# Kernel optimization log

Measured on AMD Instinct MI355X. Metric: run time of the kernel, lower is better.

## Reference

```python
import jax, jax.numpy as jnp
import numpy as np

H = 12
D_K = 64
NEG = -1e9
EPS = 1e-6
SQRT_2_PI = float(np.sqrt(2.0 / np.pi))


def gelu_tanh(x):
    return 0.5 * x * (1.0 + jnp.tanh(SQRT_2_PI * (x + 0.044715 * x * x * x)))


def layernorm(x, a, b):
    # torch std is unbiased (ddof=1); note original adds eps to std, not var
    mean = jnp.mean(x, axis=-1, keepdims=True)
    n = x.shape[-1]
    var = jnp.sum((x - mean) ** 2, axis=-1, keepdims=True) / (n - 1)
    std = jnp.sqrt(var)
    return a * (x - mean) / (std + EPS) + b


def setup_inputs() -> dict:
    key = jax.random.key(0)
    ks = jax.random.split(key, 16)
    B, S, D, F = 8, 1024, 768, 3072
    s = 0.02
    inp = {
        "x": jax.random.normal(ks[0], (B, S, D), jnp.float32),
        "mask": jnp.ones((B, 1, 1, S), jnp.int32),
        "Wq": jax.random.normal(ks[1], (D, D), jnp.float32) * s,
        "bq": jnp.zeros((D,), jnp.float32),
        "Wk": jax.random.normal(ks[2], (D, D), jnp.float32) * s,
        "bk": jnp.zeros((D,), jnp.float32),
        "Wv": jax.random.normal(ks[3], (D, D), jnp.float32) * s,
        "bv": jnp.zeros((D,), jnp.float32),
        "Wo": jax.random.normal(ks[4], (D, D), jnp.float32) * s,
        "bo": jnp.zeros((D,), jnp.float32),
        "W1": jax.random.normal(ks[5], (D, F), jnp.float32) * s,
        "b1": jnp.zeros((F,), jnp.float32),
        "W2": jax.random.normal(ks[6], (F, D), jnp.float32) * s,
        "b2": jnp.zeros((D,), jnp.float32),
        "ln1_a": jnp.ones((D,), jnp.float32),
        "ln1_b": jnp.ones((D,), jnp.float32),
        "ln2_a": jnp.ones((D,), jnp.float32),
        "ln2_b": jnp.ones((D,), jnp.float32),
    }
    return inp


def reference(x, mask, Wq, bq, Wk, bk, Wv, bv, Wo, bo, W1, b1, W2, b2,
              ln1_a, ln1_b, ln2_a, ln2_b):
    B, S, D = x.shape
    # QKV projections -> [B, H, S, d_k]
    def split_heads(t):
        return t.reshape(B, S, H, D_K).transpose(0, 2, 1, 3)
    q = split_heads(x @ Wq + bq)
    k = split_heads(x @ Wk + bk)
    v = split_heads(x @ Wv + bv)
    scores = jnp.einsum("bhqd,bhkd->bhqk", q, k) / jnp.sqrt(jnp.float32(D_K))
    scores = jnp.where(mask == 0, jnp.float32(NEG), scores)
    p = jax.nn.softmax(scores, axis=-1)
    attn = jnp.einsum("bhqk,bhkd->bhqd", p, v)
    attn = attn.transpose(0, 2, 1, 3).reshape(B, S, D)
    attn_out = attn @ Wo + bo
    out1 = layernorm(x + attn_out, ln1_a, ln1_b)
    ffn = gelu_tanh(out1 @ W1 + b1) @ W2 + b2
    out2 = layernorm(out1 + ffn, ln2_a, ln2_b)
    return out2
```

## Files before the change

kernel.cpp:

```cpp
#include <hip/hip_runtime.h>
#include <hip/hip_bf16.h>
#include <math.h>

#define BB 8
#define SS 1024
#define DD 768
#define FF 3072
#define HH 12
#define DK 64

typedef __bf16 bf16;
typedef __attribute__((ext_vector_type(8))) __bf16 bf16x8;
typedef __attribute__((ext_vector_type(4))) __bf16 bf16x4;
typedef __attribute__((ext_vector_type(4))) float f32x4;

#define AS1 __attribute__((address_space(1)))
#define AS3 __attribute__((address_space(3)))

#define EXP2_SCALE 0.18033688011112042f
#define NLOG2E2    -2.8853900817779268f

__device__ __forceinline__ float gelu_fast(float x) {
    const float u = 0.7978845608028654f * (x + 0.044715f * x * x * x);
    const float e = __builtin_amdgcn_exp2f(u * NLOG2E2);
    return x * __builtin_amdgcn_rcpf(1.0f + e);
}

template<int BN, int OUTB, int GELU_F, int RESID>
__global__ __launch_bounds__(256) void gemm_bf16(
    const bf16* __restrict__ A, const bf16* __restrict__ Bt,
    const float* __restrict__ bias, const float* __restrict__ R,
    void* __restrict__ Cout, int M, int N, int K)
{
    constexpr int NTJ   = BN / 32;
    constexpr int BITER = (BN * 8) / 256;

    __shared__ bf16x8 As[1024];
    __shared__ bf16x8 Bs[BN * 8];

    const int t    = threadIdx.x;
    const int wave = t >> 6;
    const int lane = t & 63;
    const int mtiles = M >> 7;
    const int m0 = (blockIdx.x % mtiles) * 128;
    const int n0 = (blockIdx.x / mtiles) * BN;
    const int wm = (wave >> 1) * 64;
    const int wn = (wave & 1) * (BN / 2);
    const int col  = lane & 15;
    const int quad = lane >> 4;

    f32x4 acc[4][NTJ] = {};

    const bf16* Abase = A  + (size_t)m0 * K;
    const bf16* Bbase = Bt + (size_t)n0 * K;

    for (int k0 = 0; k0 < K; k0 += 64) {
        if (k0) __syncthreads();

        #pragma unroll
        for (int i = 0; i < 4; ++i) {
            const int chunk = i * 256 + wave * 64 + lane;
            const int r  = chunk >> 3;
            const int kc = (chunk & 7) ^ (r & 7);
            const bf16* ga = Abase + (size_t)r * K + k0 + kc * 8;
            __builtin_amdgcn_global_load_lds((AS1 void*)ga, (AS3 void*)(As + i * 256 + wave * 64), 16, 0, 0);
        }
        #pragma unroll
        for (int i = 0; i < BITER; ++i) {
            const int chunk = i * 256 + wave * 64 + lane;
            const int r  = chunk >> 3;
            const int kc = (chunk & 7) ^ (r & 7);
            const bf16* gb = Bbase + (size_t)r * K + k0 + kc * 8;
            __builtin_amdgcn_global_load_lds((AS1 void*)gb, (AS3 void*)(Bs + i * 256 + wave * 64), 16, 0, 0);
        }
        __syncthreads();

        const bf16* Asp = (const bf16*)As;
        const bf16* Bsp = (const bf16*)Bs;
        #pragma unroll
        for (int ks = 0; ks < 2; ++ks) {
            bf16x8 af[4], bfr[NTJ];
            #pragma unroll
            for (int ti = 0; ti < 4; ++ti) {
                const int r  = wm + ti * 16 + col;
                const int cs = (ks * 4 + quad) ^ (r & 7);
                af[ti] = *(const bf16x8*)(Asp + r * 64 + cs * 8);
            }
            #pragma unroll
            for (int tj = 0; tj < NTJ; ++tj) {
                const int r  = wn + tj * 16 + col;
                const int cs = (ks * 4 + quad) ^ (r & 7);
                bfr[tj] = *(const bf16x8*)(Bsp + r * 64 + cs * 8);
            }
            #pragma unroll
            for (int ti = 0; ti < 4; ++ti)
                #pragma unroll
                for (int tj = 0; tj < NTJ; ++tj)
                    acc[ti][tj] = __builtin_amdgcn_mfma_f32_16x16x32_bf16(
                        af[ti], bfr[tj], acc[ti][tj], 0, 0, 0);
        }
    }

    float biasv[NTJ];
    #pragma unroll
    for (int tj = 0; tj < NTJ; ++tj) biasv[tj] = bias[n0 + wn + tj * 16 + col];

    #pragma unroll
    for (int ti = 0; ti < 4; ++ti) {
        #pragma unroll
        for (int tj = 0; tj < NTJ; ++tj) {
            const int n = n0 + wn + tj * 16 + col;
            #pragma unroll
            for (int i = 0; i < 4; ++i) {
                const int m = m0 + wm + ti * 16 + quad * 4 + i;
                float v = acc[ti][tj][i] + biasv[tj];
                if (GELU_F) v = gelu_fast(v);
                if (RESID) v += R[(size_t)m * N + n];
                if (OUTB) ((bf16*)Cout)[(size_t)m * N + n] = (bf16)v;
                else      ((float*)Cout)[(size_t)m * N + n] = v;
            }
        }
    }
}

__device__ __forceinline__ void tc32(
    const float* __restrict__ src, bf16* __restrict__ dst,
    int R, int C, int c0, int r0, int t)
{
    __shared__ float tile[32][33];
    const int tx = t & 31, ty = t >> 5;
    #pragma unroll
    for (int i = 0; i < 32; i += 8)
        tile[ty + i][tx] = src[(size_t)(r0 + ty + i) * C + c0 + tx];
    __syncthreads();
    #pragma unroll
    for (int i = 0; i < 32; i += 8)
        dst[(size_t)(c0 + ty + i) * R + r0 + tx] = (bf16)tile[tx][ty + i];
}

__global__ __launch_bounds__(256) void prep_all(
    const float* __restrict__ Wq, const float* __restrict__ Wk,
    const float* __restrict__ Wv, const float* __restrict__ Wo,
    const float* __restrict__ W1, const float* __restrict__ W2,
    const float* __restrict__ bq, const float* __restrict__ bk,
    const float* __restrict__ bv, const float* __restrict__ x,
    bf16* __restrict__ wqkvb, bf16* __restrict__ wob,
    bf16* __restrict__ wt1b,  bf16* __restrict__ wt2b,
    float* __restrict__ bqkv, bf16x4* __restrict__ xb)
{
    const int blk = blockIdx.x;
    const int t = threadIdx.x;
    if (blk < 2304) {
        const int job = blk / 576, loc = blk % 576;
        const int c0 = (loc % 24) * 32, r0 = (loc / 24) * 32;
        const float* src = (job == 0) ? Wq : (job == 1) ? Wk : (job == 2) ? Wv : Wo;
        bf16* dst = (job == 3) ? wob : wqkvb + (size_t)job * DD * DD;
        tc32(src, dst, DD, DD, c0, r0, t);
    } else if (blk < 4608) {
        const int loc = blk - 2304;
        tc32(W1, wt1b, DD, FF, (loc % 96) * 32, (loc / 96) * 32, t);
    } else if (blk < 6912) {
        const int loc = blk - 4608;
        tc32(W2, wt2b, FF, DD, (loc % 24) * 32, (loc / 24) * 32, t);
    } else if (blk < 6921) {
        const int i = (blk - 6912) * 256 + t;
        if (i < 3 * DD)
            bqkv[i] = (i < DD) ? bq[i] : (i < 2 * DD ? bk[i - DD] : bv[i - 2 * DD]);
    } else {
        const int i = (blk - 6921) * 256 + t;
        const float4 v = ((const float4*)x)[i];
        bf16x4 o;
        o.x = (bf16)v.x; o.y = (bf16)v.y; o.z = (bf16)v.z; o.w = (bf16)v.w;
        xb[i] = o;
    }
}

__global__ __launch_bounds__(256) void vtrans(
    const bf16* __restrict__ qkvb, bf16* __restrict__ vtb)
{
    __shared__ bf16 tile[32][33];
    const int s0 = blockIdx.x * 32, d0 = blockIdx.y * 32;
    const int bh = blockIdx.z;
    const int b = bh / HH, h = bh % HH;
    const int tx = threadIdx.x & 31, ty = threadIdx.x >> 5;
    #pragma unroll
    for (int i = 0; i < 32; i += 8)
        tile[ty + i][tx] = qkvb[(size_t)(b * SS + s0 + ty + i) * 2304 + 1536 + h * DK + d0 + tx];
    __syncthreads();
    #pragma unroll
    for (int i = 0; i < 32; i += 8)
        vtb[(size_t)(bh * DK + d0 + ty + i) * SS + s0 + tx] = tile[tx][ty + i];
}

__global__ __launch_bounds__(256) void flash_mfma(
    const bf16* __restrict__ qkvb,
    const bf16* __restrict__ vtb,
    const int*  __restrict__ mask,
    bf16* __restrict__ O)
{
    __shared__ bf16x8 Ks[512];
    __shared__ bf16x8 Vs[512];
    __shared__ bf16   Ps[4 * 32 * 64];

    const int t    = threadIdx.x;
    const int wave = t >> 6;
    const int lane = t & 63;
    const int col  = lane & 15;
    const int quad = lane >> 4;
    const int bh = blockIdx.x % (BB * HH);
    const int q0 = (blockIdx.x / (BB * HH)) * 128;
    const int b  = bh / HH;
    const int h  = bh % HH;

    bf16x8 aq[2][2];
    #pragma unroll
    for (int mi = 0; mi < 2; ++mi)
        #pragma unroll
        for (int ks = 0; ks < 2; ++ks)
            aq[mi][ks] = *(const bf16x8*)(qkvb
                + (size_t)(b * SS + q0 + wave * 32 + mi * 16 + col) * 2304
                + h * DK + ks * 32 + quad * 8);

    f32x4 o[2][4] = {};
    float l_part[2][4] = {};

    bf16* Pw = Ps + wave * 2048;

    for (int c0 = 0; c0 < SS; c0 += 64) {
        if (c0) __syncthreads();

        #pragma unroll
        for (int i = 0; i < 2; ++i) {
            const int s  = i * 256 + wave * 64 + lane;
            const int r  = s >> 3;
            const int kc = (s & 7) ^ (r & 7);
            const bf16* gk = qkvb + (size_t)(b * SS + c0 + r) * 2304 + DD + h * DK + kc * 8;
            __builtin_amdgcn_global_load_lds((AS1 void*)gk, (AS3 void*)(Ks + i * 256 + wave * 64), 16, 0, 0);
            const bf16* gv = vtb + (size_t)(bh * DK + r) * SS + c0 + kc * 8;
            __builtin_amdgcn_global_load_lds((AS1 void*)gv, (AS3 void*)(Vs + i * 256 + wave * 64), 16, 0, 0);
        }
        __syncthreads();

        const bf16* Ksp = (const bf16*)Ks;
        f32x4 s4[2][4] = {};
        {
            bf16x8 kf[2][4];
            #pragma unroll
            for (int ks = 0; ks < 2; ++ks)
                #pragma unroll
                for (int tj = 0; tj < 4; ++tj) {
                    const int r  = tj * 16 + col;
                    const int sl = (ks * 4 + quad) ^ (r & 7);
                    kf[ks][tj] = *(const bf16x8*)(Ksp + r * 64 + sl * 8);
                }
            #pragma unroll
            for (int mi = 0; mi < 2; ++mi)
                #pragma unroll
                for (int ks = 0; ks < 2; ++ks)
                    #pragma unroll
                    for (int tj = 0; tj < 4; ++tj)
                        s4[mi][tj] = __builtin_amdgcn_mfma_f32_16x16x32_bf16(
                            aq[mi][ks], kf[ks][tj], s4[mi][tj], 0, 0, 0);
        }

        int mk[4];
        #pragma unroll
        for (int tj = 0; tj < 4; ++tj) mk[tj] = mask[b * SS + c0 + tj * 16 + col];

        #pragma unroll
        for (int mi = 0; mi < 2; ++mi)
            #pragma unroll
            for (int i = 0; i < 4; ++i) {
                const int rf = mi * 16 + quad * 4 + i;
                #pragma unroll
                for (int tj = 0; tj < 4; ++tj) {
                    const float sv = (mk[tj] == 0) ? -1e9f : s4[mi][tj][i];
                    const float p = __builtin_amdgcn_exp2f(sv * EXP2_SCALE);
                    l_part[mi][i] += p;
                    const int c  = tj * 16 + col;
                    const int sl = ((c >> 3) ^ (rf & 7));
                    Pw[rf * 64 + sl * 8 + (c & 7)] = (bf16)p;
                }
            }

        const bf16* Vsp = (const bf16*)Vs;
        bf16x8 vf[2][4];
        #pragma unroll
        for (int ks = 0; ks < 2; ++ks)
            #pragma unroll
            for (int tj = 0; tj < 4; ++tj) {
                const int r  = tj * 16 + col;
                const int sl = (ks * 4 + quad) ^ (r & 7);
                vf[ks][tj] = *(const bf16x8*)(Vsp + r * 64 + sl * 8);
            }
        #pragma unroll
        for (int mi = 0; mi < 2; ++mi) {
            bf16x8 pf[2];
            #pragma unroll
            for (int ks = 0; ks < 2; ++ks) {
                const int rf = mi * 16 + col;
                const int sl = (ks * 4 + quad) ^ (rf & 7);
                pf[ks] = *(const bf16x8*)(Pw + rf * 64 + sl * 8);
            }
            #pragma unroll
            for (int ks = 0; ks < 2; ++ks)
                #pragma unroll
                for (int tj = 0; tj < 4; ++tj)
                    o[mi][tj] = __builtin_amdgcn_mfma_f32_16x16x32_bf16(
                        pf[ks], vf[ks][tj], o[mi][tj], 0, 0, 0);
        }
    }

    #pragma unroll
    for (int mi = 0; mi < 2; ++mi)
        #pragma unroll
        for (int i = 0; i < 4; ++i) {
            float l = l_part[mi][i];
            #pragma unroll
            for (int off = 1; off < 16; off <<= 1)
                l += __shfl_xor(l, off, 64);
            const float inv = 1.0f / l;
            const int q = q0 + wave * 32 + mi * 16 + quad * 4 + i;
            #pragma unroll
            for (int tj = 0; tj < 4; ++tj)
                O[(size_t)(b * SS + q) * DD + h * DK + tj * 16 + col] =
                    (bf16)(o[mi][tj][i] * inv);
        }
}

__global__ __launch_bounds__(256) void layernorm_k(
    const float* __restrict__ X,
    const float* __restrict__ ga, const float* __restrict__ gb,
    float* __restrict__ out, bf16* __restrict__ outb)
{
    __shared__ float red[4];
    const int row = blockIdx.x;
    const int t   = threadIdx.x;
    const float* x = X + (size_t)row * DD;

    float v[3];
    #pragma unroll
    for (int i = 0; i < 3; ++i) v[i] = x[t + i * 256];

    float s = v[0] + v[1] + v[2];
    #pragma unroll
    for (int off = 32; off > 0; off >>= 1) s += __shfl_down(s, off, 64);
    if ((t & 63) == 0) red[t >> 6] = s;
    __syncthreads();
    const float mean = (red[0] + red[1] + red[2] + red[3]) * (1.0f / 768.0f);
    __syncthreads();

    float sq = 0.f;
    #pragma unroll
    for (int i = 0; i < 3; ++i) { const float d = v[i] - mean; sq += d * d; }
    #pragma unroll
    for (int off = 32; off > 0; off >>= 1) sq += __shfl_down(sq, off, 64);
    if ((t & 63) == 0) red[t >> 6] = sq;
    __syncthreads();
    const float var = (red[0] + red[1] + red[2] + red[3]) * (1.0f / 767.0f);
    const float inv = 1.0f / (sqrtf(var) + 1e-6f);

    #pragma unroll
    for (int i = 0; i < 3; ++i) {
        const int c = t + i * 256;
        const float r = ga[c] * (v[i] - mean) * inv + gb[c];
        out[(size_t)row * DD + c] = r;
        if (outb) outb[(size_t)row * DD + c] = (bf16)r;
    }
}

extern "C" void kernel_launch(void* const* d_in, const int* in_sizes, int n_in,
                              void* d_out, int out_size, void* d_ws, size_t ws_size,
                              hipStream_t stream)
{
    const float* x    = (const float*)d_in[0];
    const int*   mask = (const int*)  d_in[1];
    const float* Wq   = (const float*)d_in[2];
    const float* bq   = (const float*)d_in[3];
    const float* Wk   = (const float*)d_in[4];
    const float* bk   = (const float*)d_in[5];
    const float* Wv   = (const float*)d_in[6];
    const float* bv   = (const float*)d_in[7];
    const float* Wo   = (const float*)d_in[8];
    const float* bo   = (const float*)d_in[9];
    const float* W1   = (const float*)d_in[10];
    const float* b1   = (const float*)d_in[11];
    const float* W2   = (const float*)d_in[12];
    const float* b2   = (const float*)d_in[13];
    const float* ln1a = (const float*)d_in[14];
    const float* ln1b = (const float*)d_in[15];
    const float* ln2a = (const float*)d_in[16];
    const float* ln2b = (const float*)d_in[17];
    float* out = (float*)d_out;

    const int M = BB * SS;
    const size_t nBSD = (size_t)M * DD;

    char* w = (char*)d_ws;
    bf16*  qkvb  = (bf16*)w;            w += (size_t)M * 3 * DD * 2;
    bf16*  vtb   = (bf16*)w;            w += (size_t)BB * HH * DK * SS * 2;
    bf16*  attnb = (bf16*)w;            w += nBSD * 2;
    float* attn_sum = (float*)w;        w += nBSD * 4;
    float* out1  = (float*)w;           w += nBSD * 4;
    float* ffn_sum = (float*)w;         w += nBSD * 4;
    bf16*  xb    = (bf16*)w;            w += nBSD * 2;
    bf16*  hbuf  = (bf16*)w;            w += (size_t)M * FF * 2;
    bf16*  wqkvb = (bf16*)w;            w += (size_t)3 * DD * DD * 2;
    bf16*  wob   = (bf16*)w;            w += (size_t)DD * DD * 2;
    bf16*  wt1b  = (bf16*)w;            w += (size_t)DD * FF * 2;
    bf16*  wt2b  = (bf16*)w;            w += (size_t)FF * DD * 2;
    float* bqkv  = (float*)w;           w += (size_t)3 * DD * 4;
    bf16*  out1b = xb;

    const dim3 blk(256);

    prep_all<<<dim3(13065), blk, 0, stream>>>(
        Wq, Wk, Wv, Wo, W1, W2, bq, bk, bv, x,
        wqkvb, wob, wt1b, wt2b, bqkv, (bf16x4*)xb);

    gemm_bf16<128, 1, 0, 0><<<dim3((M / 128) * (3 * DD / 128)), blk, 0, stream>>>(
        xb, wqkvb, bqkv, nullptr, qkvb, M, 3 * DD, DD);

    vtrans<<<dim3(SS / 32, DK / 32, BB * HH), blk, 0, stream>>>(qkvb, vtb);

    flash_mfma<<<dim3((SS / 128) * BB * HH), blk, 0, stream>>>(qkvb, vtb, mask, attnb);

    gemm_bf16<64, 0, 0, 1><<<dim3((M / 128) * (DD / 64)), blk, 0, stream>>>(
        attnb, wob, bo, x, attn_sum, M, DD, DD);

    layernorm_k<<<dim3(M), blk, 0, stream>>>(attn_sum, ln1a, ln1b, out1, out1b);

    gemm_bf16<128, 1, 1, 0><<<dim3((M / 128) * (FF / 128)), blk, 0, stream>>>(
        out1b, wt1b, b1, nullptr, hbuf, M, FF, DD);

    gemm_bf16<64, 0, 0, 1><<<dim3((M / 128) * (DD / 64)), blk, 0, stream>>>(
        hbuf, wt2b, b2, out1, ffn_sum, M, DD, FF);

    layernorm_k<<<dim3(M), blk, 0, stream>>>(ffn_sum, ln2a, ln2b, out, nullptr);
}
```

Baseline: 370.9 us.

## Double-buffer K/V tiles in flash attention and prefetch next chunk

The attention kernel now keeps two LDS buffers for K and V and issues the async global-to-LDS loads for the next 64-key chunk before computing on the current one, so memory latency overlaps with MFMA and softmax work. The mask is turned into an additive bias folded into an FMA before exp2, and s_setprio wraps the MFMA blocks to favour matrix issue. LDS use grows by another K/V pair, which may lower occupancy. There is still only one barrier per iteration, and it sits at the end of the loop; it is unclear whether the prefetched buffer is reliably complete before the next iteration reads it, since no explicit wait on the async loads is visible.

```diff
diff --git a/kernel.cpp b/kernel.cpp
--- a/kernel.cpp
+++ b/kernel.cpp
@@ -19,6 +19,7 @@
 
 #define EXP2_SCALE 0.18033688011112042f
 #define NLOG2E2    -2.8853900817779268f
+#define MASK_BIAS  -1.8033688e8f
 
 __device__ __forceinline__ float gelu_fast(float x) {
     const float u = 0.7978845608028654f * (x + 0.044715f * x * x * x);
@@ -198,8 +199,8 @@
     const int*  __restrict__ mask,
     bf16* __restrict__ O)
 {
-    __shared__ bf16x8 Ks[512];
-    __shared__ bf16x8 Vs[512];
+    __shared__ bf16x8 Ks[2][512];
+    __shared__ bf16x8 Vs[2][512];
     __shared__ bf16   Ps[4 * 32 * 64];
 
     const int t    = threadIdx.x;
@@ -226,22 +227,36 @@
 
     bf16* Pw = Ps + wave * 2048;
 
-    for (int c0 = 0; c0 < SS; c0 += 64) {
-        if (c0) __syncthreads();
-
+    auto stage = [&](int buf, int c0) {
         #pragma unroll
         for (int i = 0; i < 2; ++i) {
             const int s  = i * 256 + wave * 64 + lane;
             const int r  = s >> 3;
             const int kc = (s & 7) ^ (r & 7);
             const bf16* gk = qkvb + (size_t)(b * SS + c0 + r) * 2304 + DD + h * DK + kc * 8;
-            __builtin_amdgcn_global_load_lds((AS1 void*)gk, (AS3 void*)(Ks + i * 256 + wave * 64), 16, 0, 0);
+            __builtin_amdgcn_global_load_lds((AS1 void*)gk,
+                (AS3 void*)(&Ks[buf][i * 256 + wave * 64]), 16, 0, 0);
             const bf16* gv = vtb + (size_t)(bh * DK + r) * SS + c0 + kc * 8;
-            __builtin_amdgcn_global_load_lds((AS1 void*)gv, (AS3 void*)(Vs + i * 256 + wave * 64), 16, 0, 0);
-        }
-        __syncthreads();
-
-        const bf16* Ksp = (const bf16*)Ks;
+            __builtin_amdgcn_global_load_lds((AS1 void*)gv,
+                (AS3 void*)(&Vs[buf][i * 256 + wave * 64]), 16, 0, 0);
+        }
+    };
+
+    stage(0, 0);
+    __syncthreads();
+
+    for (int it = 0; it < SS / 64; ++it) {
+        const int cur = it & 1;
+        const int c0  = it * 64;
+
+        if (it + 1 < SS / 64) stage(cur ^ 1, c0 + 64);
+
+        float mb[4];
+        #pragma unroll
+        for (int tj = 0; tj < 4; ++tj)
+            mb[tj] = (mask[b * SS + c0 + tj * 16 + col] == 0) ? MASK_BIAS : 0.0f;
+
+        const bf16* Ksp = (const bf16*)Ks[cur];
         f32x4 s4[2][4] = {};
         {
             bf16x8 kf[2][4];
@@ -253,6 +268,7 @@
                     const int sl = (ks * 4 + quad) ^ (r & 7);
                     kf[ks][tj] = *(const bf16x8*)(Ksp + r * 64 + sl * 8);
                 }
+            __builtin_amdgcn_s_setprio(1);
             #pragma unroll
             for (int mi = 0; mi < 2; ++mi)
                 #pragma unroll
@@ -261,11 +277,8 @@
                     for (int tj = 0; tj < 4; ++tj)
                         s4[mi][tj] = __builtin_amdgcn_mfma_f32_16x16x32_bf16(
                             aq[mi][ks], kf[ks][tj], s4[mi][tj], 0, 0, 0);
-        }
-
-        int mk[4];
-        #pragma unroll
-        for (int tj = 0; tj < 4; ++tj) mk[tj] = mask[b * SS + c0 + tj * 16 + col];
+            __builtin_amdgcn_s_setprio(0);
+        }
 
         #pragma unroll
         for (int mi = 0; mi < 2; ++mi)
@@ -274,8 +287,8 @@
                 const int rf = mi * 16 + quad * 4 + i;
                 #pragma unroll
                 for (int tj = 0; tj < 4; ++tj) {
-                    const float sv = (mk[tj] == 0) ? -1e9f : s4[mi][tj][i];
-                    const float p = __builtin_amdgcn_exp2f(sv * EXP2_SCALE);
+                    const float p = __builtin_amdgcn_exp2f(
+                        __builtin_fmaf(s4[mi][tj][i], EXP2_SCALE, mb[tj]));
                     l_part[mi][i] += p;
                     const int c  = tj * 16 + col;
                     const int sl = ((c >> 3) ^ (rf & 7));
@@ -283,7 +296,7 @@
                 }
             }
 
-        const bf16* Vsp = (const bf16*)Vs;
+        const bf16* Vsp = (const bf16*)Vs[cur];
         bf16x8 vf[2][4];
         #pragma unroll
         for (int ks = 0; ks < 2; ++ks)
@@ -302,13 +315,17 @@
                 const int sl = (ks * 4 + quad) ^ (rf & 7);
                 pf[ks] = *(const bf16x8*)(Pw + rf * 64 + sl * 8);
             }
+            __builtin_amdgcn_s_setprio(1);
             #pragma unroll
             for (int ks = 0; ks < 2; ++ks)
                 #pragma unroll
                 for (int tj = 0; tj < 4; ++tj)
                     o[mi][tj] = __builtin_amdgcn_mfma_f32_16x16x32_bf16(
                         pf[ks], vf[ks][tj], o[mi][tj], 0, 0, 0);
-        }
+            __builtin_amdgcn_s_setprio(0);
+        }
+
+        __syncthreads();
     }
 
     #pragma unroll
```

Result: slower. 384.8 us (+3.7%).

## Load K/V fragments directly from global in flash attention, precompute mask bias in LDS

Applied to the files above, without the earlier changes.

The flash attention kernel stops staging K and V tiles in shared memory through global_load_lds and block barriers. Each wave now reads its MFMA fragments straight from global memory and relies on cache hits, since all four waves read the same K/V. The mask is turned once per block into an additive bias held in LDS and folded into the exp2 argument with an fma, which replaces the per-iteration mask load and select. This removes the per-tile __syncthreads and LDS staging, but it adds repeated, less coalesced global loads: K rows have a 2304-element stride, and each wave refetches the same data.

```diff
diff --git a/kernel.cpp b/kernel.cpp
--- a/kernel.cpp
+++ b/kernel.cpp
@@ -19,6 +19,7 @@
 
 #define EXP2_SCALE 0.18033688011112042f
 #define NLOG2E2    -2.8853900817779268f
+#define MASK_BIAS  -1.8033688e8f
 
 __device__ __forceinline__ float gelu_fast(float x) {
     const float u = 0.7978845608028654f * (x + 0.044715f * x * x * x);
@@ -198,9 +199,8 @@
     const int*  __restrict__ mask,
     bf16* __restrict__ O)
 {
-    __shared__ bf16x8 Ks[512];
-    __shared__ bf16x8 Vs[512];
-    __shared__ bf16   Ps[4 * 32 * 64];
+    __shared__ bf16  Ps[4 * 32 * 64];
+    __shared__ float Mb[SS];
 
     const int t    = threadIdx.x;
     const int wave = t >> 6;
@@ -212,6 +212,12 @@
     const int b  = bh / HH;
     const int h  = bh % HH;
 
+    #pragma unroll
+    for (int i = 0; i < 4; ++i) {
+        const int c = t + i * 256;
+        Mb[c] = (mask[b * SS + c] == 0) ? MASK_BIAS : 0.0f;
+    }
+
     bf16x8 aq[2][2];
     #pragma unroll
     for (int mi = 0; mi < 2; ++mi)
@@ -221,51 +227,47 @@
                 + (size_t)(b * SS + q0 + wave * 32 + mi * 16 + col) * 2304
                 + h * DK + ks * 32 + quad * 8);
 
+    __syncthreads();
+
+    const bf16* Kg = qkvb + (size_t)b * SS * 2304 + DD + h * DK;
+    const bf16* Vg = vtb + (size_t)bh * DK * SS;
+
     f32x4 o[2][4] = {};
     float l_part[2][4] = {};
-
     bf16* Pw = Ps + wave * 2048;
 
-    for (int c0 = 0; c0 < SS; c0 += 64) {
-        if (c0) __syncthreads();
-
-        #pragma unroll
-        for (int i = 0; i < 2; ++i) {
-            const int s  = i * 256 + wave * 64 + lane;
-            const int r  = s >> 3;
-            const int kc = (s & 7) ^ (r & 7);
-            const bf16* gk = qkvb + (size_t)(b * SS + c0 + r) * 2304 + DD + h * DK + kc * 8;
-            __builtin_amdgcn_global_load_lds((AS1 void*)gk, (AS3 void*)(Ks + i * 256 + wave * 64), 16, 0, 0);
-            const bf16* gv = vtb + (size_t)(bh * DK + r) * SS + c0 + kc * 8;
-            __builtin_amdgcn_global_load_lds((AS1 void*)gv, (AS3 void*)(Vs + i * 256 + wave * 64), 16, 0, 0);
-        }
-        __syncthreads();
-
-        const bf16* Ksp = (const bf16*)Ks;
+    for (int it = 0; it < SS / 64; ++it) {
+        const int c0 = it * 64;
+
+        bf16x8 kf[2][4];
+        #pragma unroll
+        for (int ks = 0; ks < 2; ++ks)
+            #pragma unroll
+            for (int tj = 0; tj < 4; ++tj)
+                kf[ks][tj] = *(const bf16x8*)(Kg
+                    + (size_t)(c0 + tj * 16 + col) * 2304 + ks * 32 + quad * 8);
+
         f32x4 s4[2][4] = {};
-        {
-            bf16x8 kf[2][4];
+        #pragma unroll
+        for (int mi = 0; mi < 2; ++mi)
             #pragma unroll
             for (int ks = 0; ks < 2; ++ks)
                 #pragma unroll
-                for (int tj = 0; tj < 4; ++tj) {
-                    const int r  = tj * 16 + col;
-                    const int sl = (ks * 4 + quad) ^ (r & 7);
-                    kf[ks][tj] = *(const bf16x8*)(Ksp + r * 64 + sl * 8);
-                }
-            #pragma unroll
-            for (int mi = 0; mi < 2; ++mi)
-                #pragma unroll
-                for (int ks = 0; ks < 2; ++ks)
-                    #pragma unroll
-                    for (int tj = 0; tj < 4; ++tj)
-                        s4[mi][tj] = __builtin_amdgcn_mfma_f32_16x16x32_bf16(
-                            aq[mi][ks], kf[ks][tj], s4[mi][tj], 0, 0, 0);
-        }
-
-        int mk[4];
-        #pragma unroll
-        for (int tj = 0; tj < 4; ++tj) mk[tj] = mask[b * SS + c0 + tj * 16 + col];
+                for (int tj = 0; tj < 4; ++tj)
+                    s4[mi][tj] = __builtin_amdgcn_mfma_f32_16x16x32_bf16(
+                        aq[mi][ks], kf[ks][tj], s4[mi][tj], 0, 0, 0);
+
+        bf16x8 vf[2][4];
+        #pragma unroll
+        for (int ks = 0; ks < 2; ++ks)
+            #pragma unroll
+            for (int tj = 0; tj < 4; ++tj)
+                vf[ks][tj] = *(const bf16x8*)(Vg
+                    + (size_t)(tj * 16 + col) * SS + c0 + ks * 32 + quad * 8);
+
+        float mbv[4];
+        #pragma unroll
+        for (int tj = 0; tj < 4; ++tj) mbv[tj] = Mb[c0 + tj * 16 + col];
 
         #pragma unroll
         for (int mi = 0; mi < 2; ++mi)
@@ -274,8 +276,8 @@
                 const int rf = mi * 16 + quad * 4 + i;
                 #pragma unroll
                 for (int tj = 0; tj < 4; ++tj) {
-                    const float sv = (mk[tj] == 0) ? -1e9f : s4[mi][tj][i];
-                    const float p = __builtin_amdgcn_exp2f(sv * EXP2_SCALE);
+                    const float p = __builtin_amdgcn_exp2f(
+                        __builtin_fmaf(s4[mi][tj][i], EXP2_SCALE, mbv[tj]));
                     l_part[mi][i] += p;
                     const int c  = tj * 16 + col;
                     const int sl = ((c >> 3) ^ (rf & 7));
@@ -283,16 +285,6 @@
                 }
             }
 
-        const bf16* Vsp = (const bf16*)Vs;
-        bf16x8 vf[2][4];
-        #pragma unroll
-        for (int ks = 0; ks < 2; ++ks)
-            #pragma unroll
-            for (int tj = 0; tj < 4; ++tj) {
-                const int r  = tj * 16 + col;
-                const int sl = (ks * 4 + quad) ^ (r & 7);
-                vf[ks][tj] = *(const bf16x8*)(Vsp + r * 64 + sl * 8);
-            }
         #pragma unroll
         for (int mi = 0; mi < 2; ++mi) {
             bf16x8 pf[2];
```

After: 407.3 us. +9.8%, slower.
